# Performance work log

Measured on AMD Instinct MI355X. Metric: run time of the kernel, lower is better.

Reference implementation:

```python
import jax, jax.numpy as jnp
import numpy as np

EPS = 1e-5

def _layernorm(x, g, b):
    mu = jnp.mean(x, axis=-1, keepdims=True)
    var = jnp.mean(jnp.square(x - mu), axis=-1, keepdims=True)
    return (x - mu) * jax.lax.rsqrt(var + EPS) * g + b

def _mlp(x, w1, b1, w2, b2):
    h = jax.nn.gelu(jnp.einsum('bnd,dh->bnh', x, w1) + b1, approximate=False)
    return jnp.einsum('bnh,hd->bnd', h, w2) + b2

def setup_inputs() -> dict:
    key = jax.random.key(0)
    B, N, D, H = 2, 8192, 1024, 4096
    ks = jax.random.split(key, 12)
    s1 = 1.0 / np.sqrt(D)
    s2 = 1.0 / np.sqrt(H)
    return {
        'x': jax.random.normal(ks[0], (B, N, D), dtype=jnp.float32),
        'mask': jax.random.randint(ks[1], (B, N), 0, 2) > 0,
        'g_rgb': jnp.ones((D,), jnp.float32),
        'b_rgb': jnp.zeros((D,), jnp.float32),
        'w1_rgb': jax.random.normal(ks[2], (D, H), dtype=jnp.float32) * s1,
        'b1_rgb': jnp.zeros((H,), jnp.float32),
        'w2_rgb': jax.random.normal(ks[3], (H, D), dtype=jnp.float32) * s2,
        'b2_rgb': jnp.zeros((D,), jnp.float32),
        'g_expr': jnp.ones((D,), jnp.float32),
        'b_expr': jnp.zeros((D,), jnp.float32),
        'w1_expr': jax.random.normal(ks[4], (D, H), dtype=jnp.float32) * s1,
        'b1_expr': jnp.zeros((H,), jnp.float32),
        'w2_expr': jax.random.normal(ks[5], (H, D), dtype=jnp.float32) * s2,
        'b2_expr': jnp.zeros((D,), jnp.float32),
    }

def reference(x, mask, g_rgb, b_rgb, w1_rgb, b1_rgb, w2_rgb, b2_rgb,
              g_expr, b_expr, w1_expr, b1_expr, w2_expr, b2_expr):
    # Per-token routing: rgb expert where mask, expr expert where ~mask.
    # LayerNorm+MLP are pointwise per token, so dense compute + select is
    # mathematically identical to the torch gather->compute->scatter.
    z_rgb = _mlp(_layernorm(x, g_rgb, b_rgb), w1_rgb, b1_rgb, w2_rgb, b2_rgb)
    z_expr = _mlp(_layernorm(x, g_expr, b_expr), w1_expr, b1_expr, w2_expr, b2_expr)
    z = jnp.where(mask[..., None], z_rgb, z_expr)
    return z.astype(jnp.float16)  # torch scatters into a float16 buffer
```

## Files before the change

### kernel.cpp

```cpp
#include <hip/hip_runtime.h>
#include <hip/hip_bf16.h>
#include <hip/hip_fp16.h>

#define D_ 1024
#define H_ 4096
#define NTOK 16384
#define MPAD 16640

typedef __attribute__((ext_vector_type(8))) short bf16x8;
typedef __attribute__((ext_vector_type(4))) float f32x4;

static __device__ __forceinline__ unsigned short f2bf(float f) {
  union { float f; unsigned u; } x; x.f = f;
  unsigned u = x.u + 0x7fffu + ((x.u >> 16) & 1u);
  return (unsigned short)(u >> 16);
}

static __device__ __forceinline__ void gld16(const void* g, void* l) {
  __builtin_amdgcn_global_load_lds(
      (const __attribute__((address_space(1))) unsigned int*)g,
      (__attribute__((address_space(3))) unsigned int*)l, 16, 0, 0);
}

static __device__ __forceinline__ float gelu_fast(float x) {
  const float z = x * (1.5957691216f + 0.0713548163f * x * x);
  return x * __builtin_amdgcn_rcpf(1.0f + __expf(-z));
}

__global__ __launch_bounds__(256) void transpose4_kernel(
    const float* __restrict__ w1r, const float* __restrict__ w1e,
    const float* __restrict__ w2r, const float* __restrict__ w2e,
    unsigned short* __restrict__ o1r, unsigned short* __restrict__ o1e,
    unsigned short* __restrict__ o2r, unsigned short* __restrict__ o2e,
    const int* __restrict__ mask, int* __restrict__ perm, int* __restrict__ counts) {
  __shared__ union SMem {
    float tile[64][65];
    struct { int sm[NTOK]; int wsum[4]; } c;
  } u;
  const int t = blockIdx.x;
  if (t == 4096) {
    const int NT = 256, CH = NTOK / NT;
    const int tt = threadIdx.x;
    const int ln = tt & 63, wv = tt >> 6;
    for (int i = tt; i < NTOK; i += NT) u.c.sm[i] = mask[i];
    for (int i = tt; i < MPAD; i += NT) perm[i] = -1;
    __syncthreads();
    const int base = tt * CH;
    int cnt = 0;
    for (int i = 0; i < CH; ++i) cnt += (u.c.sm[base + i] != 0);
    int sc = cnt;
#pragma unroll
    for (int o = 1; o < 64; o <<= 1) {
      int up = __shfl_up(sc, o, 64);
      if (ln >= o) sc += up;
    }
    if (ln == 63) u.c.wsum[wv] = sc;
    __syncthreads();
    int woff = 0;
#pragma unroll
    for (int j = 0; j < 4; ++j) woff += (j < wv) ? u.c.wsum[j] : 0;
    const int total1 = u.c.wsum[0] + u.c.wsum[1] + u.c.wsum[2] + u.c.wsum[3];
    if (tt == 0) { counts[0] = total1; counts[1] = NTOK - total1; }
    const int excl = woff + sc - cnt;
    const int expr_base = ((total1 + 255) >> 8) << 8;
    int p1 = excl;
    int p0 = expr_base + (base - excl);
    for (int i = 0; i < CH; ++i) {
      const int idx = base + i;
      if (u.c.sm[idx] != 0) perm[p1++] = idx; else perm[p0++] = idx;
    }
    return;
  }
  const float* src; unsigned short* dst; int R, C, tl;
  if (t < 1024)       { src = w1r; dst = o1r; R = D_; C = H_; tl = t; }
  else if (t < 2048)  { src = w1e; dst = o1e; R = D_; C = H_; tl = t - 1024; }
  else if (t < 3072)  { src = w2r; dst = o2r; R = H_; C = D_; tl = t - 2048; }
  else                { src = w2e; dst = o2e; R = H_; C = D_; tl = t - 3072; }
  const int tc = C >> 6;
  const int r0 = (tl / tc) * 64, c0 = (tl % tc) * 64;
  const int tx = threadIdx.x & 63, ty = threadIdx.x >> 6;
#pragma unroll
  for (int i = 0; i < 64; i += 4)
    u.tile[ty + i][tx] = src[(size_t)(r0 + ty + i) * C + c0 + tx];
  __syncthreads();
  const int wl = threadIdx.x & 31, wrow = threadIdx.x >> 5;
#pragma unroll
  for (int i = 0; i < 64; i += 8) {
    const int orow = wrow + i;
    const unsigned lo = f2bf(u.tile[2 * wl][orow]);
    const unsigned hi = f2bf(u.tile[2 * wl + 1][orow]);
    *(unsigned*)(dst + (size_t)(c0 + orow) * R + r0 + 2 * wl) = lo | (hi << 16);
  }
}

__global__ __launch_bounds__(512) void ln_kernel(
    const float* __restrict__ x, const int* __restrict__ mask,
    const int* __restrict__ perm,
    const float* __restrict__ g_rgb, const float* __restrict__ b_rgb,
    const float* __restrict__ g_expr, const float* __restrict__ b_expr,
    unsigned short* __restrict__ xln) {
  const int h = threadIdx.x >> 8;
  const int tid = threadIdx.x & 255;
  const int i = blockIdx.x * 2 + h;
  int t = perm[i];
  const bool live = t >= 0;
  if (!live) t = 0;
  const float4 v = ((const float4*)(x + (size_t)t * D_))[tid];
  float s = v.x + v.y + v.z + v.w;
  float ss = v.x * v.x + v.y * v.y + v.z * v.z + v.w * v.w;
#pragma unroll
  for (int o = 32; o > 0; o >>= 1) {
    s += __shfl_xor(s, o, 64);
    ss += __shfl_xor(ss, o, 64);
  }
  __shared__ float red[16];
  const int wv = threadIdx.x >> 6, ln = threadIdx.x & 63;
  if (ln == 0) { red[wv] = s; red[8 + wv] = ss; }
  __syncthreads();
  const int rb = h * 4;
  s = red[rb + 0] + red[rb + 1] + red[rb + 2] + red[rb + 3];
  ss = red[8 + rb + 0] + red[8 + rb + 1] + red[8 + rb + 2] + red[8 + rb + 3];
  const float mu = s * (1.0f / D_);
  const float var = ss * (1.0f / D_) - mu * mu;
  const float rs = rsqrtf(var + 1e-5f);
  const bool rgb = mask[t] != 0;
  const float4 gv = ((const float4*)(rgb ? g_rgb : g_expr))[tid];
  const float4 bv = ((const float4*)(rgb ? b_rgb : b_expr))[tid];
  const unsigned short o0 = f2bf((v.x - mu) * rs * gv.x + bv.x);
  const unsigned short o1 = f2bf((v.y - mu) * rs * gv.y + bv.y);
  const unsigned short o2 = f2bf((v.z - mu) * rs * gv.z + bv.z);
  const unsigned short o3 = f2bf((v.w - mu) * rs * gv.w + bv.w);
  uint2 pk;
  pk.x = (unsigned)o0 | ((unsigned)o1 << 16);
  pk.y = (unsigned)o2 | ((unsigned)o3 << 16);
  if (live) *((uint2*)(xln + (size_t)i * D_ + tid * 4)) = pk;
}

template <int K, int N>
__global__ __launch_bounds__(512, 2) void gemm8_kernel(
    const unsigned short* __restrict__ A,
    const unsigned short* __restrict__ Wt_rgb,
    const unsigned short* __restrict__ Wt_expr,
    const float* __restrict__ bias_rgb,
    const float* __restrict__ bias_expr,
    const int* __restrict__ counts,
    unsigned short* __restrict__ Out) {
  constexpr int MT = MPAD / 256;
  constexpr int NT = N / 256;
  constexpr int ntk = K / 64;
  constexpr int KH2 = 128 * K * 2;

  const int tid = threadIdx.x;
  const int id = blockIdx.x;
  const int xcd = id & 7;
  const int slot = id >> 3;
  const int p = xcd * ((MT * NT) / 8) + slot;
  const int m0 = (p / NT) * 256;
  const int n0 = (p % NT) * 256;
  const int cnt_rgb = counts[0];
  const unsigned short* Wt = (m0 < cnt_rgb) ? Wt_rgb : Wt_expr;
  const float* bias = (m0 < cnt_rgb) ? bias_rgb : bias_expr;

  __shared__ unsigned short As[2][256 * 64];
  __shared__ unsigned short Bs[2][256 * 64];

  const int lane = tid & 63, wave = tid >> 6;
  const int wr = wave >> 2, wc = wave & 3;
  const int quad = lane >> 4, l16 = lane & 15;

  f32x4 acc[8][4] = {};

  const char* Abase = (const char*)A;
  const char* Wbase = (const char*)Wt;

  int agK0, agK1, bgK0, bgK1, sl0, sl1;
  {
    const int s0 = tid, s1 = 512 + tid;
    const int r0 = s0 >> 3, r1 = s1 >> 3;
    const int ks0 = ((s0 ^ r0) & 7) * 8, ks1 = ((s1 ^ r1) & 7) * 8;
    agK0 = ((m0 + r0) * K + ks0) * 2;  agK1 = ((m0 + r1) * K + ks1) * 2;
    bgK0 = ((n0 + r0) * K + ks0) * 2;  bgK1 = ((n0 + r1) * K + ks1) * 2;
    sl0 = s0 * 16;  sl1 = s1 * 16;
  }

  int aoffL[2][2][4];
  int boffL[2][4];
#pragma unroll
  for (int kk = 0; kk < 2; ++kk) {
    const int cb = kk * 4 + quad;
#pragma unroll
    for (int mh = 0; mh < 2; ++mh)
#pragma unroll
      for (int mi = 0; mi < 4; ++mi) {
        const int row = wr * 128 + mh * 64 + mi * 16 + l16;
        aoffL[kk][mh][mi] = (row * 64 + ((cb ^ row) & 7) * 8) * 2;
      }
#pragma unroll
    for (int ni = 0; ni < 4; ++ni) {
      const int row = wc * 64 + ni * 16 + l16;
      boffL[kk][ni] = (row * 64 + ((cb ^ row) & 7) * 8) * 2;
    }
  }

  bf16x8 aX0, aX1, aX2, aX3, aY0, aY1, aY2, aY3;
  bf16x8 b00, b01, b02, b03, b10, b11, b12, b13;

#define STAGE_A(T1, HA, Q) do { \
    gld16(Abase + agK0 + (HA) * KH2 + (T1) * 128, (char*)As + (Q) * 32768 + (HA) * 16384 + sl0); \
    gld16(Abase + agK1 + (HA) * KH2 + (T1) * 128, (char*)As + (Q) * 32768 + (HA) * 16384 + sl1); \
  } while (0)
#define STAGE_B(T2, HB, Q) do { \
    gld16(Wbase + bgK0 + (HB) * KH2 + (T2) * 128, (char*)Bs + (Q) * 32768 + (HB) * 16384 + sl0); \
    gld16(Wbase + bgK1 + (HB) * KH2 + (T2) * 128, (char*)Bs + (Q) * 32768 + (HB) * 16384 + sl1); \
  } while (0)
#define RD_A4(D0, D1, D2, D3, P_, KK, MH) do { \
    const char* _ab = (const char*)As + (P_) * 32768; \
    D0 = *(const bf16x8*)(_ab + aoffL[KK][MH][0]); \
    D1 = *(const bf16x8*)(_ab + aoffL[KK][MH][1]); \
    D2 = *(const bf16x8*)(_ab + aoffL[KK][MH][2]); \
    D3 = *(const bf16x8*)(_ab + aoffL[KK][MH][3]); \
  } while (0)
#define RD_B4(D0, D1, D2, D3, P_, KK) do { \
    const char* _bp = (const char*)Bs + (P_) * 32768; \
    D0 = *(const bf16x8*)(_bp + boffL[KK][0]); \
    D1 = *(const bf16x8*)(_bp + boffL[KK][1]); \
    D2 = *(const bf16x8*)(_bp + boffL[KK][2]); \
    D3 = *(const bf16x8*)(_bp + boffL[KK][3]); \
  } while (0)
#define MFMA16(A0_, A1_, A2_, A3_, B0_, B1_, B2_, B3_, MO) do { \
    acc[(MO)+0][0] = __builtin_amdgcn_mfma_f32_16x16x32_bf16(A0_, B0_, acc[(MO)+0][0], 0, 0, 0); \
    acc[(MO)+0][1] = __builtin_amdgcn_mfma_f32_16x16x32_bf16(A0_, B1_, acc[(MO)+0][1], 0, 0, 0); \
    acc[(MO)+0][2] = __builtin_amdgcn_mfma_f32_16x16x32_bf16(A0_, B2_, acc[(MO)+0][2], 0, 0, 0); \
    acc[(MO)+0][3] = __builtin_amdgcn_mfma_f32_16x16x32_bf16(A0_, B3_, acc[(MO)+0][3], 0, 0, 0); \
    acc[(MO)+1][0] = __builtin_amdgcn_mfma_f32_16x16x32_bf16(A1_, B0_, acc[(MO)+1][0], 0, 0, 0); \
    acc[(MO)+1][1] = __builtin_amdgcn_mfma_f32_16x16x32_bf16(A1_, B1_, acc[(MO)+1][1], 0, 0, 0); \
    acc[(MO)+1][2] = __builtin_amdgcn_mfma_f32_16x16x32_bf16(A1_, B2_, acc[(MO)+1][2], 0, 0, 0); \
    acc[(MO)+1][3] = __builtin_amdgcn_mfma_f32_16x16x32_bf16(A1_, B3_, acc[(MO)+1][3], 0, 0, 0); \
    acc[(MO)+2][0] = __builtin_amdgcn_mfma_f32_16x16x32_bf16(A2_, B0_, acc[(MO)+2][0], 0, 0, 0); \
    acc[(MO)+2][1] = __builtin_amdgcn_mfma_f32_16x16x32_bf16(A2_, B1_, acc[(MO)+2][1], 0, 0, 0); \
    acc[(MO)+2][2] = __builtin_amdgcn_mfma_f32_16x16x32_bf16(A2_, B2_, acc[(MO)+2][2], 0, 0, 0); \
    acc[(MO)+2][3] = __builtin_amdgcn_mfma_f32_16x16x32_bf16(A2_, B3_, acc[(MO)+2][3], 0, 0, 0); \
    acc[(MO)+3][0] = __builtin_amdgcn_mfma_f32_16x16x32_bf16(A3_, B0_, acc[(MO)+3][0], 0, 0, 0); \
    acc[(MO)+3][1] = __builtin_amdgcn_mfma_f32_16x16x32_bf16(A3_, B1_, acc[(MO)+3][1], 0, 0, 0); \
    acc[(MO)+3][2] = __builtin_amdgcn_mfma_f32_16x16x32_bf16(A3_, B2_, acc[(MO)+3][2], 0, 0, 0); \
    acc[(MO)+3][3] = __builtin_amdgcn_mfma_f32_16x16x32_bf16(A3_, B3_, acc[(MO)+3][3], 0, 0, 0); \
  } while (0)

#define KTILE(P_, T1_, ST_) do { \
    if (ST_) { \
      STAGE_A(T1_, 0, (P_) ^ 1); STAGE_A(T1_, 1, (P_) ^ 1); \
      STAGE_B(T1_, 0, (P_) ^ 1); STAGE_B(T1_, 1, (P_) ^ 1); \
    } \
    RD_B4(b00, b01, b02, b03, P_, 0); \
    RD_A4(aX0, aX1, aX2, aX3, P_, 0, 0); \
    RD_A4(aY0, aY1, aY2, aY3, P_, 0, 1); \
    RD_B4(b10, b11, b12, b13, P_, 1); \
    __builtin_amdgcn_s_setprio(1); \
    MFMA16(aX0, aX1, aX2, aX3, b00, b01, b02, b03, 0); \
    __builtin_amdgcn_s_setprio(0); \
    RD_A4(aX0, aX1, aX2, aX3, P_, 1, 0); \
    __builtin_amdgcn_s_setprio(1); \
    MFMA16(aY0, aY1, aY2, aY3, b00, b01, b02, b03, 4); \
    __builtin_amdgcn_s_setprio(0); \
    RD_A4(aY0, aY1, aY2, aY3, P_, 1, 1); \
    __builtin_amdgcn_s_setprio(1); \
    MFMA16(aX0, aX1, aX2, aX3, b10, b11, b12, b13, 0); \
    MFMA16(aY0, aY1, aY2, aY3, b10, b11, b12, b13, 4); \
    __builtin_amdgcn_s_setprio(0); \
    __syncthreads(); \
  } while (0)

  STAGE_A(0, 0, 0); STAGE_A(0, 1, 0);
  STAGE_B(0, 0, 0); STAGE_B(0, 1, 0);
  __syncthreads();

  for (int tt = 0; tt < ntk / 2; ++tt) {
    KTILE(0, 2 * tt + 1, 1);
    KTILE(1, 2 * tt + 2, tt < ntk / 2 - 1);
  }

#undef KTILE
#undef MFMA16
#undef RD_B4
#undef RD_A4
#undef STAGE_B
#undef STAGE_A

  float bv[4];
#pragma unroll
  for (int ni = 0; ni < 4; ++ni) bv[ni] = bias[n0 + wc * 64 + ni * 16 + l16];
#pragma unroll
  for (int mi = 0; mi < 8; ++mi) {
#pragma unroll
    for (int r = 0; r < 4; ++r) {
      const int row = m0 + wr * 128 + mi * 16 + quad * 4 + r;
      unsigned short* orow = Out + (size_t)row * N + n0 + wc * 64 + l16;
#pragma unroll
      for (int ni = 0; ni < 4; ++ni)
        orow[ni * 16] = f2bf(gelu_fast(acc[mi][ni][r] + bv[ni]));
    }
  }
}

template <int EP, int K, int N>
__global__ __launch_bounds__(256) void gemm_kernel(
    const unsigned short* __restrict__ A,
    const unsigned short* __restrict__ Wt_rgb,
    const unsigned short* __restrict__ Wt_expr,
    const float* __restrict__ bias_rgb,
    const float* __restrict__ bias_expr,
    const int* __restrict__ counts,
    const int* __restrict__ perm,
    void* __restrict__ OutP,
    const int mbase) {
  constexpr int BM = 128, BN = 128, BK = 64;
  constexpr int MTH = (MPAD / 2) / BM;
  constexpr int NT = N / BN;
  const int tid = threadIdx.x;
  const int id = blockIdx.x;
  const int xcd = id & 7;
  const int slot = id >> 3;
  const int p = xcd * ((MTH * NT) / 8) + slot;
  const int m0 = mbase + (p / NT) * BM;
  const int n0 = (p % NT) * BN;
  const int cnt_rgb = counts[0];
  const unsigned short* Wt = (m0 < cnt_rgb) ? Wt_rgb : Wt_expr;
  const float* bias = (m0 < cnt_rgb) ? bias_rgb : bias_expr;

  __shared__ unsigned short As[BM * BK];
  __shared__ unsigned short Bs[BN * BK];

  f32x4 acc[4][4] = {};

  const int lane = tid & 63, wave = tid >> 6;
  const int wm = (wave & 1) * 64, wn = (wave >> 1) * 64;
  const int quad = lane >> 4, l16 = lane & 15;

  const char* Abase = (const char*)A;
  const char* Wbase = (const char*)Wt;
  const char* AsB = (const char*)As;
  const char* BsB = (const char*)Bs;

  int ag[4], bg[4], sl[4];
#pragma unroll
  for (int it = 0; it < 4; ++it) {
    const int s = it * 256 + tid;
    const int row = s >> 3;
    const int ks = ((s ^ row) & 7) * 8;
    ag[it] = ((m0 + row) * K + ks) * 2;
    bg[it] = ((n0 + row) * K + ks) * 2;
    sl[it] = s * 16;
  }
  int aoff[2][4], boff[2][4];
#pragma unroll
  for (int hh = 0; hh < 2; ++hh) {
    const int cb = hh * 4 + quad;
#pragma unroll
    for (int mi = 0; mi < 4; ++mi) {
      const int row = wm + mi * 16 + l16;
      aoff[hh][mi] = (row * BK + (((cb ^ row) & 7) << 3)) * 2;
    }
#pragma unroll
    for (int ni = 0; ni < 4; ++ni) {
      const int row = wn + ni * 16 + l16;
      boff[hh][ni] = (row * BK + (((cb ^ row) & 7) << 3)) * 2;
    }
  }

  for (int k0 = 0; k0 < K; k0 += BK) {
#pragma unroll
    for (int it = 0; it < 4; ++it) {
      gld16(Abase + ag[it], (void*)(AsB + sl[it]));
      gld16(Wbase + bg[it], (void*)(BsB + sl[it]));
      ag[it] += BK * 2;
      bg[it] += BK * 2;
    }
    __syncthreads();
#pragma unroll
    for (int hh = 0; hh < 2; ++hh) {
      bf16x8 a[4], b[4];
#pragma unroll
      for (int mi = 0; mi < 4; ++mi) a[mi] = *(const bf16x8*)(AsB + aoff[hh][mi]);
#pragma unroll
      for (int ni = 0; ni < 4; ++ni) b[ni] = *(const bf16x8*)(BsB + boff[hh][ni]);
#pragma unroll
      for (int mi = 0; mi < 4; ++mi)
#pragma unroll
        for (int ni = 0; ni < 4; ++ni)
          acc[mi][ni] = __builtin_amdgcn_mfma_f32_16x16x32_bf16(a[mi], b[ni], acc[mi][ni], 0, 0, 0);
    }
    __syncthreads();
  }

  float bv[4];
#pragma unroll
  for (int ni = 0; ni < 4; ++ni) bv[ni] = bias[n0 + wn + ni * 16 + l16];

#pragma unroll
  for (int mi = 0; mi < 4; ++mi) {
#pragma unroll
    for (int r = 0; r < 4; ++r) {
      const int row = m0 + wm + mi * 16 + quad * 4 + r;
      if (EP == 0) {
        unsigned short* orow = (unsigned short*)OutP + (size_t)row * N + n0 + wn + l16;
#pragma unroll
        for (int ni = 0; ni < 4; ++ni) {
          orow[ni * 16] = f2bf(gelu_fast(acc[mi][ni][r] + bv[ni]));
        }
      } else {
        const int p2 = perm[row];
        if (p2 < 0) continue;
        float* orow = (float*)OutP + (size_t)p2 * N + n0 + wn + l16;
#pragma unroll
        for (int ni = 0; ni < 4; ++ni) {
          float v = acc[mi][ni][r] + bv[ni];
          orow[ni * 16] = __half2float(__float2half_rn(v));
        }
      }
    }
  }
}

extern "C" void kernel_launch(void* const* d_in, const int* in_sizes, int n_in,
                              void* d_out, int out_size, void* d_ws, size_t ws_size,
                              hipStream_t stream) {
  const float* x       = (const float*)d_in[0];
  const int*   mask    = (const int*)d_in[1];
  const float* g_rgb   = (const float*)d_in[2];
  const float* b_rgb   = (const float*)d_in[3];
  const float* w1_rgb  = (const float*)d_in[4];
  const float* b1_rgb  = (const float*)d_in[5];
  const float* w2_rgb  = (const float*)d_in[6];
  const float* b2_rgb  = (const float*)d_in[7];
  const float* g_expr  = (const float*)d_in[8];
  const float* b_expr  = (const float*)d_in[9];
  const float* w1_expr = (const float*)d_in[10];
  const float* b1_expr = (const float*)d_in[11];
  const float* w2_expr = (const float*)d_in[12];
  const float* b2_expr = (const float*)d_in[13];

  char* w = (char*)d_ws;
  int* counts               = (int*)(w + 0);
  int* perm                 = (int*)(w + 256);
  unsigned short* w1t_rgb   = (unsigned short*)(w + 66816);
  unsigned short* w1t_expr  = (unsigned short*)(w + 8455424);
  unsigned short* w2t_rgb   = (unsigned short*)(w + 16844032);
  unsigned short* w2t_expr  = (unsigned short*)(w + 25232640);
  unsigned short* xln       = (unsigned short*)(w + 33621248);
  unsigned short* h         = (unsigned short*)(w + 67699968);

  transpose4_kernel<<<4097, 256, 0, stream>>>(
      w1_rgb, w1_expr, w2_rgb, w2_expr, w1t_rgb, w1t_expr, w2t_rgb, w2t_expr,
      mask, perm, counts);

  ln_kernel<<<MPAD / 2, 512, 0, stream>>>(x, mask, perm, g_rgb, b_rgb, g_expr, b_expr, xln);

  gemm8_kernel<D_, H_><<<dim3((MPAD / 256) * (H_ / 256)), 512, 0, stream>>>(
      xln, w1t_rgb, w1t_expr, b1_rgb, b1_expr, counts, h);

  gemm_kernel<1, H_, D_><<<dim3((D_ / 128) * (MPAD / 2 / 128)), 256, 0, stream>>>(
      h, w2t_rgb, w2t_expr, b2_rgb, b2_expr, counts, perm, d_out, 0);
  gemm_kernel<1, H_, D_><<<dim3((D_ / 128) * (MPAD / 2 / 128)), 256, 0, stream>>>(
      h, w2t_rgb, w2t_expr, b2_rgb, b2_expr, counts, perm, d_out, MPAD / 2);
}
```

Baseline: 587.9 us.

## Double-buffer LDS in second GEMM and merge its two launches into one

Rewrites the second GEMM's K loop to use two LDS buffers. The next K-tile's global-to-LDS loads are issued before computing on the current one, with one barrier per tile instead of two, and MFMA priority is raised during compute. The two half-M launches are also merged into a single grid covering all of MPAD, which removes a launch and its tail. LDS use doubles to 64KB per block, which may lower occupancy.

```diff
diff --git a/kernel.cpp b/kernel.cpp
--- a/kernel.cpp
+++ b/kernel.cpp
@@ -302,8 +302,8 @@
   }
 }
 
-template <int EP, int K, int N>
-__global__ __launch_bounds__(256) void gemm_kernel(
+template <int K, int N>
+__global__ __launch_bounds__(256) void gemm2_kernel(
     const unsigned short* __restrict__ A,
     const unsigned short* __restrict__ Wt_rgb,
     const unsigned short* __restrict__ Wt_expr,
@@ -311,24 +311,24 @@
     const float* __restrict__ bias_expr,
     const int* __restrict__ counts,
     const int* __restrict__ perm,
-    void* __restrict__ OutP,
-    const int mbase) {
+    float* __restrict__ Out) {
   constexpr int BM = 128, BN = 128, BK = 64;
-  constexpr int MTH = (MPAD / 2) / BM;
+  constexpr int MT = MPAD / BM;
   constexpr int NT = N / BN;
+  constexpr int ntk = K / BK;
   const int tid = threadIdx.x;
   const int id = blockIdx.x;
   const int xcd = id & 7;
   const int slot = id >> 3;
-  const int p = xcd * ((MTH * NT) / 8) + slot;
-  const int m0 = mbase + (p / NT) * BM;
+  const int p = xcd * ((MT * NT) / 8) + slot;
+  const int m0 = (p / NT) * BM;
   const int n0 = (p % NT) * BN;
   const int cnt_rgb = counts[0];
   const unsigned short* Wt = (m0 < cnt_rgb) ? Wt_rgb : Wt_expr;
   const float* bias = (m0 < cnt_rgb) ? bias_rgb : bias_expr;
 
-  __shared__ unsigned short As[BM * BK];
-  __shared__ unsigned short Bs[BN * BK];
+  __shared__ unsigned short As[2][BM * BK];
+  __shared__ unsigned short Bs[2][BN * BK];
 
   f32x4 acc[4][4] = {};
 
@@ -338,8 +338,6 @@
 
   const char* Abase = (const char*)A;
   const char* Wbase = (const char*)Wt;
-  const char* AsB = (const char*)As;
-  const char* BsB = (const char*)Bs;
 
   int ag[4], bg[4], sl[4];
 #pragma unroll
@@ -367,30 +365,78 @@
     }
   }
 
-  for (int k0 = 0; k0 < K; k0 += BK) {
-#pragma unroll
-    for (int it = 0; it < 4; ++it) {
-      gld16(Abase + ag[it], (void*)(AsB + sl[it]));
-      gld16(Wbase + bg[it], (void*)(BsB + sl[it]));
-      ag[it] += BK * 2;
-      bg[it] += BK * 2;
-    }
-    __syncthreads();
-#pragma unroll
-    for (int hh = 0; hh < 2; ++hh) {
-      bf16x8 a[4], b[4];
-#pragma unroll
-      for (int mi = 0; mi < 4; ++mi) a[mi] = *(const bf16x8*)(AsB + aoff[hh][mi]);
-#pragma unroll
-      for (int ni = 0; ni < 4; ++ni) b[ni] = *(const bf16x8*)(BsB + boff[hh][ni]);
-#pragma unroll
-      for (int mi = 0; mi < 4; ++mi)
-#pragma unroll
-        for (int ni = 0; ni < 4; ++ni)
-          acc[mi][ni] = __builtin_amdgcn_mfma_f32_16x16x32_bf16(a[mi], b[ni], acc[mi][ni], 0, 0, 0);
-    }
-    __syncthreads();
-  }
+  bf16x8 aX0, aX1, aX2, aX3, aY0, aY1, aY2, aY3;
+  bf16x8 b00, b01, b02, b03, b10, b11, b12, b13;
+
+#define STAGE2(T_, Q_) do { \
+    gld16(Abase + ag[0] + (T_) * 128, (char*)As + (Q_) * 16384 + sl[0]); \
+    gld16(Abase + ag[1] + (T_) * 128, (char*)As + (Q_) * 16384 + sl[1]); \
+    gld16(Abase + ag[2] + (T_) * 128, (char*)As + (Q_) * 16384 + sl[2]); \
+    gld16(Abase + ag[3] + (T_) * 128, (char*)As + (Q_) * 16384 + sl[3]); \
+    gld16(Wbase + bg[0] + (T_) * 128, (char*)Bs + (Q_) * 16384 + sl[0]); \
+    gld16(Wbase + bg[1] + (T_) * 128, (char*)Bs + (Q_) * 16384 + sl[1]); \
+    gld16(Wbase + bg[2] + (T_) * 128, (char*)Bs + (Q_) * 16384 + sl[2]); \
+    gld16(Wbase + bg[3] + (T_) * 128, (char*)Bs + (Q_) * 16384 + sl[3]); \
+  } while (0)
+#define RD2_A(D0, D1, D2, D3, P_, KK) do { \
+    const char* _ab = (const char*)As + (P_) * 16384; \
+    D0 = *(const bf16x8*)(_ab + aoff[KK][0]); \
+    D1 = *(const bf16x8*)(_ab + aoff[KK][1]); \
+    D2 = *(const bf16x8*)(_ab + aoff[KK][2]); \
+    D3 = *(const bf16x8*)(_ab + aoff[KK][3]); \
+  } while (0)
+#define RD2_B(D0, D1, D2, D3, P_, KK) do { \
+    const char* _bp = (const char*)Bs + (P_) * 16384; \
+    D0 = *(const bf16x8*)(_bp + boff[KK][0]); \
+    D1 = *(const bf16x8*)(_bp + boff[KK][1]); \
+    D2 = *(const bf16x8*)(_bp + boff[KK][2]); \
+    D3 = *(const bf16x8*)(_bp + boff[KK][3]); \
+  } while (0)
+#define MFMA2(A0_, A1_, A2_, A3_, B0_, B1_, B2_, B3_) do { \
+    acc[0][0] = __builtin_amdgcn_mfma_f32_16x16x32_bf16(A0_, B0_, acc[0][0], 0, 0, 0); \
+    acc[0][1] = __builtin_amdgcn_mfma_f32_16x16x32_bf16(A0_, B1_, acc[0][1], 0, 0, 0); \
+    acc[0][2] = __builtin_amdgcn_mfma_f32_16x16x32_bf16(A0_, B2_, acc[0][2], 0, 0, 0); \
+    acc[0][3] = __builtin_amdgcn_mfma_f32_16x16x32_bf16(A0_, B3_, acc[0][3], 0, 0, 0); \
+    acc[1][0] = __builtin_amdgcn_mfma_f32_16x16x32_bf16(A1_, B0_, acc[1][0], 0, 0, 0); \
+    acc[1][1] = __builtin_amdgcn_mfma_f32_16x16x32_bf16(A1_, B1_, acc[1][1], 0, 0, 0); \
+    acc[1][2] = __builtin_amdgcn_mfma_f32_16x16x32_bf16(A1_, B2_, acc[1][2], 0, 0, 0); \
+    acc[1][3] = __builtin_amdgcn_mfma_f32_16x16x32_bf16(A1_, B3_, acc[1][3], 0, 0, 0); \
+    acc[2][0] = __builtin_amdgcn_mfma_f32_16x16x32_bf16(A2_, B0_, acc[2][0], 0, 0, 0); \
+    acc[2][1] = __builtin_amdgcn_mfma_f32_16x16x32_bf16(A2_, B1_, acc[2][1], 0, 0, 0); \
+    acc[2][2] = __builtin_amdgcn_mfma_f32_16x16x32_bf16(A2_, B2_, acc[2][2], 0, 0, 0); \
+    acc[2][3] = __builtin_amdgcn_mfma_f32_16x16x32_bf16(A2_, B3_, acc[2][3], 0, 0, 0); \
+    acc[3][0] = __builtin_amdgcn_mfma_f32_16x16x32_bf16(A3_, B0_, acc[3][0], 0, 0, 0); \
+    acc[3][1] = __builtin_amdgcn_mfma_f32_16x16x32_bf16(A3_, B1_, acc[3][1], 0, 0, 0); \
+    acc[3][2] = __builtin_amdgcn_mfma_f32_16x16x32_bf16(A3_, B2_, acc[3][2], 0, 0, 0); \
+    acc[3][3] = __builtin_amdgcn_mfma_f32_16x16x32_bf16(A3_, B3_, acc[3][3], 0, 0, 0); \
+  } while (0)
+
+#define KTILE2(P_, T1_, ST_) do { \
+    if (ST_) STAGE2(T1_, (P_) ^ 1); \
+    RD2_B(b00, b01, b02, b03, P_, 0); \
+    RD2_A(aX0, aX1, aX2, aX3, P_, 0); \
+    RD2_A(aY0, aY1, aY2, aY3, P_, 1); \
+    RD2_B(b10, b11, b12, b13, P_, 1); \
+    __builtin_amdgcn_s_setprio(1); \
+    MFMA2(aX0, aX1, aX2, aX3, b00, b01, b02, b03); \
+    MFMA2(aY0, aY1, aY2, aY3, b10, b11, b12, b13); \
+    __builtin_amdgcn_s_setprio(0); \
+    __syncthreads(); \
+  } while (0)
+
+  STAGE2(0, 0);
+  __syncthreads();
+
+  for (int tt = 0; tt < ntk / 2; ++tt) {
+    KTILE2(0, 2 * tt + 1, 1);
+    KTILE2(1, 2 * tt + 2, tt < ntk / 2 - 1);
+  }
+
+#undef KTILE2
+#undef MFMA2
+#undef RD2_B
+#undef RD2_A
+#undef STAGE2
 
   float bv[4];
 #pragma unroll
@@ -401,21 +447,13 @@
 #pragma unroll
     for (int r = 0; r < 4; ++r) {
       const int row = m0 + wm + mi * 16 + quad * 4 + r;
-      if (EP == 0) {
-        unsigned short* orow = (unsigned short*)OutP + (size_t)row * N + n0 + wn + l16;
-#pragma unroll
-        for (int ni = 0; ni < 4; ++ni) {
-          orow[ni * 16] = f2bf(gelu_fast(acc[mi][ni][r] + bv[ni]));
-        }
-      } else {
-        const int p2 = perm[row];
-        if (p2 < 0) continue;
-        float* orow = (float*)OutP + (size_t)p2 * N + n0 + wn + l16;
-#pragma unroll
-        for (int ni = 0; ni < 4; ++ni) {
-          float v = acc[mi][ni][r] + bv[ni];
-          orow[ni * 16] = __half2float(__float2half_rn(v));
-        }
+      const int p2 = perm[row];
+      if (p2 < 0) continue;
+      float* orow = Out + (size_t)p2 * N + n0 + wn + l16;
+#pragma unroll
+      for (int ni = 0; ni < 4; ++ni) {
+        float v = acc[mi][ni][r] + bv[ni];
+        orow[ni * 16] = __half2float(__float2half_rn(v));
       }
     }
   }
@@ -458,8 +496,6 @@
   gemm8_kernel<D_, H_><<<dim3((MPAD / 256) * (H_ / 256)), 512, 0, stream>>>(
       xln, w1t_rgb, w1t_expr, b1_rgb, b1_expr, counts, h);
 
-  gemm_kernel<1, H_, D_><<<dim3((D_ / 128) * (MPAD / 2 / 128)), 256, 0, stream>>>(
-      h, w2t_rgb, w2t_expr, b2_rgb, b2_expr, counts, perm, d_out, 0);
-  gemm_kernel<1, H_, D_><<<dim3((D_ / 128) * (MPAD / 2 / 128)), 256, 0, stream>>>(
-      h, w2t_rgb, w2t_expr, b2_rgb, b2_expr, counts, perm, d_out, MPAD / 2);
-}
+  gemm2_kernel<H_, D_><<<dim3((D_ / 128) * (MPAD / 128)), 256, 0, stream>>>(
+      h, w2t_rgb, w2t_expr, b2_rgb, b2_expr, counts, perm, (float*)d_out);
+}
```

New measurement: 584.0 us. No clear change (-0.7%).
